# Kernel tuning notes

Hardware: AMD Instinct MI355X
Metric: run time of the kernel (lower is better)

## Reference

```python
import jax, jax.numpy as jnp
import numpy as np

N_HEADS = 16
HEAD_SIZE = 128  # n_embd // n_vq_heads = 2048 // 16
N_OPTIONS = 512


def setup_inputs() -> dict:
    key = jax.random.key(0)
    k1, k2, k3 = jax.random.split(key, 3)
    B, S, E = 4, 2048, N_HEADS * HEAD_SIZE
    x = jax.random.normal(k1, (B, S, E), dtype=jnp.float32)
    vq_head_weights = jax.random.normal(k2, (N_HEADS, N_OPTIONS, HEAD_SIZE), dtype=jnp.float32)
    vq_codebooks = jax.random.normal(k3, (N_HEADS, N_OPTIONS, HEAD_SIZE), dtype=jnp.float32)
    temperature = jnp.float32(1.0)
    return {
        "x": x,
        "vq_head_weights": vq_head_weights,
        "vq_codebooks": vq_codebooks,
        "temperature": temperature,
    }


def reference(x, vq_head_weights, vq_codebooks, temperature):
    # Training-mode forward of VQizer (softmax path).
    B, S, E = x.shape
    H, O, A = vq_head_weights.shape  # heads, options, head_size
    x_prepped = x.reshape(B, S, H, A)
    # per-head logits over codebook options
    logits = jnp.einsum('bsha,hoa->bsho', x_prepped, vq_head_weights)
    probs = jax.nn.softmax(logits / temperature, axis=-1)
    out = jnp.einsum('bsho,hoa->bsha', probs, vq_codebooks)
    return out.reshape(B, S, H * A)
```

## Files before the change

### kernel.cpp

```cpp
#include <hip/hip_runtime.h>
#include <math.h>

#define NHEADS 16
#define HS     128
#define NOPT   512
#define TB     128
#define OC     32
#define NCH    16
#define NITER  8
#define EMB    2048
#define LOG2E  1.44269504088896340736f
#define THRD   11.0f

typedef short bf16x8 __attribute__((ext_vector_type(8)));
typedef _Float16 f16x8 __attribute__((ext_vector_type(8)));
typedef unsigned short u16x8 __attribute__((ext_vector_type(8)));
typedef float f32x4 __attribute__((ext_vector_type(4)));
typedef float f32x16 __attribute__((ext_vector_type(16)));
typedef unsigned u32x4 __attribute__((ext_vector_type(4)));

__device__ __forceinline__ unsigned short f2bf(float f) {
    union { float f; unsigned u; } v; v.f = f;
    unsigned r = v.u + 0x7FFFu + ((v.u >> 16) & 1u);
    return (unsigned short)(r >> 16);
}
__device__ __forceinline__ float bf2f(unsigned short h) {
    union { unsigned u; float f; } v; v.u = ((unsigned)h) << 16;
    return v.f;
}
__device__ __forceinline__ unsigned short f2h(float f) {
    const _Float16 h = (_Float16)f;
    return __builtin_bit_cast(unsigned short, h);
}
__device__ __forceinline__ void gll16(const void* gptr, void* lptr) {
    __builtin_amdgcn_global_load_lds(
        (const __attribute__((address_space(1))) void*)gptr,
        (__attribute__((address_space(3))) void*)lptr,
        16, 0, 0);
}
__device__ __forceinline__ unsigned pkrtz(float lo, float hi) {
    unsigned r;
    asm("v_cvt_pkrtz_f16_f32 %0, %1, %2" : "=v"(r) : "v"(lo), "v"(hi));
    return r;
}
__device__ __forceinline__ void pl32swap(unsigned &a, unsigned &b) {
    asm volatile("v_permlane32_swap_b32 %0, %1" : "+v"(a), "+v"(b));
}
__device__ __forceinline__ f32x16 mfma32h(f16x8 a, f16x8 b, f32x16 c) {
    return __builtin_amdgcn_mfma_f32_32x32x16_f16(a, b, c, 0, 0, 0);
}

#define WCH    4096
#define CCH    4096
#define WS_C0  (NHEADS * NCH * WCH)
#define WS_TOTAL_BYTES ((size_t)(WS_C0 + NHEADS * NCH * CCH) * 2)

__global__ __launch_bounds__(256) void vq_prep(const float* __restrict__ W,
                                               const float* __restrict__ C,
                                               const float* __restrict__ temp,
                                               unsigned short* __restrict__ ws)
{
    const int b = blockIdx.x, t = threadIdx.x;
    if (b < NHEADS * NCH) {
        const float scW = (1.0f / temp[0]) * LOG2E;
        const float* src = W + (size_t)b * OC * HS;
        unsigned short* dst = ws + (size_t)b * WCH;
        for (int k = 0; k < 16; ++k) {
            const int e = k * 256 + t;
            const int opt = e >> 7, col = e & 127;
            dst[opt * 128 + (col ^ ((opt & 15) << 3))] = f2h(src[e] * scW);
        }
    } else {
        const int b2 = b - NHEADS * NCH;
        const float* src = C + (size_t)b2 * OC * HS;
        unsigned short* dst = ws + WS_C0 + (size_t)b2 * CCH;
        for (int k = 0; k < 16; ++k) {
            const int e = k * 256 + t;
            const int opt = e >> 7, a = e & 127;
            dst[a * 32 + (opt ^ (((a >> 1) & 3) << 3))] = f2h(src[e]);
        }
    }
}

__global__ __launch_bounds__(256, 2) void vq_main(
    const float* __restrict__ x, const unsigned short* __restrict__ ws,
    float* __restrict__ out)
{
    __shared__ unsigned short wbuf[2][2 * WCH];
    __shared__ unsigned short cbuf[2][2 * CCH];

    const int t = threadIdx.x, l = t & 63, w = t >> 6;
    const int la = l & 31, hf = l >> 5;
    const int b = blockIdx.x;
    const int head = ((b & 7) << 1) | ((b >> 3) & 1);
    const int n0 = (b >> 4) * TB;

    const char* gwbase = (const char*)(ws + (size_t)(head * NCH) * WCH);
    const char* gcbase = (const char*)(ws + WS_C0 + (size_t)(head * NCH) * CCH);

    {
        const char* gw = gwbase + w * 4096 + l * 16;
        char* lw = (char*)&wbuf[0][0] + w * 4096;
        const char* gc = gcbase + w * 4096 + l * 16;
        char* lc = (char*)&cbuf[0][0] + w * 4096;
        #pragma unroll
        for (int i = 0; i < 4; ++i) { gll16(gw + i * 1024, lw + i * 1024);
                                      gll16(gc + i * 1024, lc + i * 1024); }
    }

    f16x8 xf[8];
    {
        const float* xr = x + (size_t)(n0 + w * 32 + la) * EMB + head * HS + hf * 8;
        #pragma unroll
        for (int kb = 0; kb < 8; ++kb) {
            const float4 v0 = *(const float4*)(xr + kb * 16);
            const float4 v1 = *(const float4*)(xr + kb * 16 + 4);
            const float vv[8] = {v0.x, v0.y, v0.z, v0.w, v1.x, v1.y, v1.z, v1.w};
            u16x8 hh;
            #pragma unroll
            for (int j = 0; j < 8; ++j) hh[j] = f2h(vv[j]);
            xf[kb] = __builtin_bit_cast(f16x8, hh);
        }
    }

    f32x16 O0 = (f32x16)0.0f, O1 = (f32x16)0.0f, O2 = (f32x16)0.0f, O3 = (f32x16)0.0f;
    float M = -1.0e30f, sacc = 0.0f;

    asm volatile("s_waitcnt vmcnt(0)" ::: "memory");
    __builtin_amdgcn_s_barrier();

    for (int cc = 0; cc < NITER; ++cc) {
        const int cur = cc & 1;
        if (cc + 1 < NITER) {
            const char* gw = gwbase + (size_t)(cc + 1) * 16384 + w * 4096 + l * 16;
            char* lw = (char*)&wbuf[cur ^ 1][0] + w * 4096;
            const char* gc = gcbase + (size_t)(cc + 1) * 16384 + w * 4096 + l * 16;
            char* lc = (char*)&cbuf[cur ^ 1][0] + w * 4096;
            #pragma unroll
            for (int i = 0; i < 4; ++i) { gll16(gw + i * 1024, lw + i * 1024);
                                          gll16(gc + i * 1024, lc + i * 1024); }
        }

        f32x16 s0a = (f32x16)0.0f, s0b = (f32x16)0.0f;
        f32x16 s1a = (f32x16)0.0f, s1b = (f32x16)0.0f;
        const unsigned short* wb0 = &wbuf[cur][0];
        const unsigned short* wb1 = &wbuf[cur][WCH];
        #pragma unroll
        for (int kb = 0; kb < 8; ++kb) {
            const int idx = la * 128 + ((kb * 16 + hf * 8) ^ ((la & 15) << 3));
            const f16x8 w0 = *(const f16x8*)&wb0[idx];
            const f16x8 w1 = *(const f16x8*)&wb1[idx];
            if (kb & 1) { s0b = mfma32h(w0, xf[kb], s0b); s1b = mfma32h(w1, xf[kb], s1b); }
            else        { s0a = mfma32h(w0, xf[kb], s0a); s1a = mfma32h(w1, xf[kb], s1a); }
        }
        f32x16 S0 = s0a + s0b;
        f32x16 S1 = s1a + s1b;

        float cmax = fmaxf(S0[0], S1[0]);
        #pragma unroll
        for (int i = 1; i < 16; ++i) cmax = fmaxf(fmaxf(cmax, S0[i]), S1[i]);
        cmax = fmaxf(cmax, __shfl_xor(cmax, 32));
        if (__any(cmax > M + THRD)) {
            const float Mn = fmaxf(M, cmax);
            const float fr = exp2f(M - Mn);
            M = Mn;
            sacc *= fr;
            #pragma unroll
            for (int q = 0; q < 16; ++q) {
                const int row = (q & 3) + 8 * (q >> 2) + 4 * hf;
                const float f = __shfl(fr, row);
                O0[q] *= f; O1[q] *= f; O2[q] *= f; O3[q] *= f;
            }
        }
        #pragma unroll
        for (int q = 0; q < 16; ++q) { S0[q] = exp2f(S0[q] - M); S1[q] = exp2f(S1[q] - M); }
        {
            float s8[8];
            #pragma unroll
            for (int i = 0; i < 8; ++i)
                s8[i] = (S0[2 * i] + S0[2 * i + 1]) + (S1[2 * i] + S1[2 * i + 1]);
            sacc += ((s8[0] + s8[1]) + (s8[2] + s8[3])) +
                    ((s8[4] + s8[5]) + (s8[6] + s8[7]));
        }

        unsigned pk0 = pkrtz(S0[0],  S0[1]),  pk1 = pkrtz(S0[2],  S0[3]);
        unsigned pk2 = pkrtz(S0[4],  S0[5]),  pk3 = pkrtz(S0[6],  S0[7]);
        unsigned pk4 = pkrtz(S0[8],  S0[9]),  pk5 = pkrtz(S0[10], S0[11]);
        unsigned pk6 = pkrtz(S0[12], S0[13]), pk7 = pkrtz(S0[14], S0[15]);
        pl32swap(pk0, pk2); pl32swap(pk1, pk3);
        pl32swap(pk4, pk6); pl32swap(pk5, pk7);
        const f16x8 pa0 = __builtin_bit_cast(f16x8, (u32x4){pk0, pk1, pk2, pk3});
        const f16x8 pa1 = __builtin_bit_cast(f16x8, (u32x4){pk4, pk5, pk6, pk7});
        unsigned qk0 = pkrtz(S1[0],  S1[1]),  qk1 = pkrtz(S1[2],  S1[3]);
        unsigned qk2 = pkrtz(S1[4],  S1[5]),  qk3 = pkrtz(S1[6],  S1[7]);
        unsigned qk4 = pkrtz(S1[8],  S1[9]),  qk5 = pkrtz(S1[10], S1[11]);
        unsigned qk6 = pkrtz(S1[12], S1[13]), qk7 = pkrtz(S1[14], S1[15]);
        pl32swap(qk0, qk2); pl32swap(qk1, qk3);
        pl32swap(qk4, qk6); pl32swap(qk5, qk7);
        const f16x8 pa2 = __builtin_bit_cast(f16x8, (u32x4){qk0, qk1, qk2, qk3});
        const f16x8 pa3 = __builtin_bit_cast(f16x8, (u32x4){qk4, qk5, qk6, qk7});

        const unsigned short* cb0 = &cbuf[cur][0];
        const unsigned short* cb1 = &cbuf[cur][CCH];
        #pragma unroll
        for (int nt = 0; nt < 4; ++nt) {
            const int a = nt * 32 + la;
            const int sw = ((a >> 1) & 3) << 3;
            const int i0 = a * 32 + ((hf * 8) ^ sw);
            const int i1 = a * 32 + ((16 + hf * 8) ^ sw);
            f32x16& O = (nt == 0) ? O0 : (nt == 1) ? O1 : (nt == 2) ? O2 : O3;
            O = mfma32h(pa0, *(const f16x8*)&cb0[i0], O);
            O = mfma32h(pa1, *(const f16x8*)&cb0[i1], O);
            O = mfma32h(pa2, *(const f16x8*)&cb1[i0], O);
            O = mfma32h(pa3, *(const f16x8*)&cb1[i1], O);
        }

        asm volatile("s_waitcnt vmcnt(0)" ::: "memory");
        if (cc + 1 < NITER) __builtin_amdgcn_s_barrier();
    }

    const float stot = sacc + __shfl_xor(sacc, 32);
    const float rs = 1.0f / stot;
    #pragma unroll
    for (int q = 0; q < 16; ++q) {
        const int row = (q & 3) + 8 * (q >> 2) + 4 * hf;
        const float rq = __shfl(rs, row);
        float* op = out + (size_t)(n0 + w * 32 + row) * EMB + head * HS + la;
        op[0]  = O0[q] * rq;
        op[32] = O1[q] * rq;
        op[64] = O2[q] * rq;
        op[96] = O3[q] * rq;
    }
}

__global__ __launch_bounds__(256, 2) void vq_fwd_mfma(
    const float* __restrict__ x, const float* __restrict__ W,
    const float* __restrict__ C, const float* __restrict__ temp,
    float* __restrict__ out)
{
    __shared__ unsigned short xh_lds[64 * HS];
    __shared__ unsigned short xl_lds[64 * HS];
    __shared__ unsigned short wst[2][64 * HS];
    __shared__ unsigned short p_lds[4][16 * 64];

    const int t = threadIdx.x, l = t & 63, w = t >> 6, lr = l & 15, lk = l >> 4;
    const int b = blockIdx.x;
    const int h = ((b & 7) << 1) | ((b >> 3) & 1);
    const int n0 = (b >> 4) * 64;
    const float invT = 1.0f / temp[0];

    #pragma unroll
    for (int kk = 0; kk < 4; ++kk) {
        const int g = t + 256 * kk;
        const int row = g >> 4, c8 = (g & 15) * 8;
        const float* src = x + (size_t)(n0 + row) * EMB + h * HS + c8;
        const float4 v0 = *(const float4*)src;
        const float4 v1 = *(const float4*)(src + 4);
        float vv[8] = {v0.x, v0.y, v0.z, v0.w, v1.x, v1.y, v1.z, v1.w};
        u16x8 hh, ll;
        #pragma unroll
        for (int j = 0; j < 8; ++j) {
            const unsigned short hb = f2bf(vv[j]);
            hh[j] = hb; ll[j] = f2bf(vv[j] - bf2f(hb));
        }
        const int idx = row * HS + (c8 ^ ((row & 7) << 3));
        *(u16x8*)&xh_lds[idx] = hh;
        *(u16x8*)&xl_lds[idx] = ll;
    }

    f32x4 acc[32];
    #pragma unroll
    for (int i = 0; i < 32; ++i) acc[i] = f32x4{0.f, 0.f, 0.f, 0.f};
    bf16x8 axh[4], axl[4];

    #pragma unroll
    for (int c = 0; c < 8; ++c) {
        if (c) __syncthreads();
        #pragma unroll
        for (int kk = 0; kk < 4; ++kk) {
            const int g = t + 256 * kk;
            const int row = g >> 4, c8 = (g & 15) * 8;
            const float* src = W + ((size_t)h * NOPT + c * 64 + row) * HS + c8;
            const float4 v0 = *(const float4*)src;
            const float4 v1 = *(const float4*)(src + 4);
            float vv[8] = {v0.x, v0.y, v0.z, v0.w, v1.x, v1.y, v1.z, v1.w};
            u16x8 hh, ll;
            #pragma unroll
            for (int j = 0; j < 8; ++j) {
                const unsigned short hb = f2bf(vv[j]);
                hh[j] = hb; ll[j] = f2bf(vv[j] - bf2f(hb));
            }
            const int idx = row * HS + (c8 ^ ((row & 7) << 3));
            *(u16x8*)&wst[0][idx] = hh;
            *(u16x8*)&wst[1][idx] = ll;
        }
        __syncthreads();
        if (c == 0) {
            const int arow = w * 16 + lr;
            #pragma unroll
            for (int ks = 0; ks < 4; ++ks) {
                const int ai = arow * HS + ((lk * 8 + ks * 32) ^ ((arow & 7) << 3));
                axh[ks] = *(const bf16x8*)&xh_lds[ai];
                axl[ks] = *(const bf16x8*)&xl_lds[ai];
            }
        }
        #pragma unroll
        for (int nt = 0; nt < 4; ++nt) {
            const int brow = nt * 16 + lr;
            #pragma unroll
            for (int ks = 0; ks < 4; ++ks) {
                const int bi = brow * HS + ((lk * 8 + ks * 32) ^ ((brow & 7) << 3));
                const bf16x8 bh = *(const bf16x8*)&wst[0][bi];
                const bf16x8 bl = *(const bf16x8*)&wst[1][bi];
                acc[c*4+nt] = __builtin_amdgcn_mfma_f32_16x16x32_bf16(axh[ks], bh, acc[c*4+nt], 0, 0, 0);
                acc[c*4+nt] = __builtin_amdgcn_mfma_f32_16x16x32_bf16(axl[ks], bh, acc[c*4+nt], 0, 0, 0);
                acc[c*4+nt] = __builtin_amdgcn_mfma_f32_16x16x32_bf16(axh[ks], bl, acc[c*4+nt], 0, 0, 0);
            }
        }
    }

    float mx[4], rsn[4];
    #pragma unroll
    for (int r = 0; r < 4; ++r) {
        float m = -3.0e38f;
        #pragma unroll
        for (int i = 0; i < 32; ++i) m = fmaxf(m, acc[i][r]);
        m *= invT;
        #pragma unroll
        for (int s = 1; s < 16; s <<= 1) m = fmaxf(m, __shfl_xor(m, s));
        float sum = 0.f;
        #pragma unroll
        for (int i = 0; i < 32; ++i) sum += exp2f((acc[i][r] * invT - m) * LOG2E);
        #pragma unroll
        for (int s = 1; s < 16; s <<= 1) sum += __shfl_xor(sum, s);
        mx[r] = m; rsn[r] = 1.0f / sum;
    }

    f32x4 oacc[8];
    #pragma unroll
    for (int i = 0; i < 8; ++i) oacc[i] = f32x4{0.f, 0.f, 0.f, 0.f};
    const int pr_ = t & 31, ag = t >> 5;
    #pragma unroll
    for (int c = 0; c < 8; ++c) {
        __syncthreads();
        {
            const float* c0p = C + ((size_t)h * NOPT + c * 64 + 2 * pr_) * HS + ag * 16;
            float va[16], vb[16];
            #pragma unroll
            for (int q = 0; q < 4; ++q) {
                const float4 u0 = ((const float4*)c0p)[q];
                const float4 u1 = ((const float4*)(c0p + HS))[q];
                va[q*4+0] = u0.x; va[q*4+1] = u0.y; va[q*4+2] = u0.z; va[q*4+3] = u0.w;
                vb[q*4+0] = u1.x; vb[q*4+1] = u1.y; vb[q*4+2] = u1.z; vb[q*4+3] = u1.w;
            }
            unsigned* ct32 = (unsigned*)&wst[0][0];
            #pragma unroll
            for (int j = 0; j < 16; ++j) {
                const int a = ag * 16 + j;
                const unsigned pkv = (unsigned)f2bf(va[j]) | ((unsigned)f2bf(vb[j]) << 16);
                ct32[a * 32 + (pr_ ^ ((a & 7) << 2))] = pkv;
            }
        }
        #pragma unroll
        for (int nt = 0; nt < 4; ++nt) {
            #pragma unroll
            for (int r = 0; r < 4; ++r) {
                const float p = exp2f((acc[c*4+nt][r] * invT - mx[r]) * LOG2E);
                const int prow = lk * 4 + r;
                const int pcol = nt * 16 + lr;
                p_lds[w][prow * 64 + (pcol ^ ((prow & 7) << 3))] = f2bf(p);
            }
        }
        __syncthreads();
        #pragma unroll
        for (int ks = 0; ks < 2; ++ks) {
            const int ai = lr * 64 + ((lk * 8 + ks * 32) ^ ((lr & 7) << 3));
            const bf16x8 pa = *(const bf16x8*)&p_lds[w][ai];
            #pragma unroll
            for (int nt = 0; nt < 8; ++nt) {
                const int brow = nt * 16 + lr;
                const int bi = brow * 64 + ((lk * 8 + ks * 32) ^ ((brow & 7) << 3));
                const bf16x8 cbv = *(const bf16x8*)&wst[0][bi];
                oacc[nt] = __builtin_amdgcn_mfma_f32_16x16x32_bf16(pa, cbv, oacc[nt], 0, 0, 0);
            }
        }
    }

    #pragma unroll
    for (int nt = 0; nt < 8; ++nt) {
        #pragma unroll
        for (int r = 0; r < 4; ++r) {
            const int tok = n0 + w * 16 + lk * 4 + r;
            out[(size_t)tok * EMB + h * HS + nt * 16 + lr] = oacc[nt][r] * rsn[r];
        }
    }
}

extern "C" void kernel_launch(void* const* d_in, const int* in_sizes, int n_in,
                              void* d_out, int out_size, void* d_ws, size_t ws_size,
                              hipStream_t stream) {
    const float* x = (const float*)d_in[0];
    const float* W = (const float*)d_in[1];
    const float* C = (const float*)d_in[2];
    const float* T = (const float*)d_in[3];
    float* out     = (float*)d_out;

    const int ntok = in_sizes[0] / EMB;

    if (ws_size >= WS_TOTAL_BYTES) {
        hipLaunchKernelGGL(vq_prep, dim3(NHEADS * NCH * 2), dim3(256), 0, stream,
                           W, C, T, (unsigned short*)d_ws);
        const int nblk = (ntok / TB) * NHEADS;
        hipLaunchKernelGGL(vq_main, dim3(nblk), dim3(256), 0, stream,
                           x, (const unsigned short*)d_ws, out);
    } else {
        const int nblk = (ntok / 64) * NHEADS;
        hipLaunchKernelGGL(vq_fwd_mfma, dim3(nblk), dim3(256), 0, stream,
                           x, W, C, T, out);
    }
}
```

Measured before the change: 73.76 us.

## Load MFMA fragments directly from global in fragment-major layout, drop LDS staging

The prep kernel now writes the fp16 weight and codebook images in the exact per-lane fragment order the MFMA operands need, so each lane reads one contiguous 16-byte vector per operand. The main kernel drops the double-buffered LDS staging, the global-to-LDS loads and the per-iteration barriers, and reads fragments straight from global memory through the caches. This removes LDS traffic and synchronisation and frees LDS for occupancy. The cost is that every wave re-reads the same data from L1/L2, and load latency is no longer hidden by explicit prefetching.

```diff
diff --git a/kernel.cpp b/kernel.cpp
--- a/kernel.cpp
+++ b/kernel.cpp
@@ -32,12 +32,6 @@
     const _Float16 h = (_Float16)f;
     return __builtin_bit_cast(unsigned short, h);
 }
-__device__ __forceinline__ void gll16(const void* gptr, void* lptr) {
-    __builtin_amdgcn_global_load_lds(
-        (const __attribute__((address_space(1))) void*)gptr,
-        (__attribute__((address_space(3))) void*)lptr,
-        16, 0, 0);
-}
 __device__ __forceinline__ unsigned pkrtz(float lo, float hi) {
     unsigned r;
     asm("v_cvt_pkrtz_f16_f32 %0, %1, %2" : "=v"(r) : "v"(lo), "v"(hi));
@@ -50,10 +44,9 @@
     return __builtin_amdgcn_mfma_f32_32x32x16_f16(a, b, c, 0, 0, 0);
 }
 
-#define WCH    4096
-#define CCH    4096
-#define WS_C0  (NHEADS * NCH * WCH)
-#define WS_TOTAL_BYTES ((size_t)(WS_C0 + NHEADS * NCH * CCH) * 2)
+#define SUBELEMS 4096
+#define WS_C0  (NHEADS * NCH * SUBELEMS)
+#define WS_TOTAL_BYTES ((size_t)(WS_C0 + NHEADS * NCH * SUBELEMS) * 2)
 
 __global__ __launch_bounds__(256) void vq_prep(const float* __restrict__ W,
                                                const float* __restrict__ C,
@@ -64,20 +57,24 @@
     if (b < NHEADS * NCH) {
         const float scW = (1.0f / temp[0]) * LOG2E;
         const float* src = W + (size_t)b * OC * HS;
-        unsigned short* dst = ws + (size_t)b * WCH;
-        for (int k = 0; k < 16; ++k) {
-            const int e = k * 256 + t;
-            const int opt = e >> 7, col = e & 127;
-            dst[opt * 128 + (col ^ ((opt & 15) << 3))] = f2h(src[e] * scW);
+        unsigned short* dst = ws + (size_t)b * SUBELEMS;
+        for (int k4 = 0; k4 < 16; ++k4) {
+            const int e = k4 * 256 + t;
+            const int opt = e >> 7, k = e & 127;
+            const int kb = k >> 4, hf = (k >> 3) & 1, j = k & 7;
+            const int l = hf * 32 + opt;
+            dst[kb * 512 + l * 8 + j] = f2h(src[e] * scW);
         }
     } else {
         const int b2 = b - NHEADS * NCH;
         const float* src = C + (size_t)b2 * OC * HS;
-        unsigned short* dst = ws + WS_C0 + (size_t)b2 * CCH;
-        for (int k = 0; k < 16; ++k) {
-            const int e = k * 256 + t;
+        unsigned short* dst = ws + WS_C0 + (size_t)b2 * SUBELEMS;
+        for (int k4 = 0; k4 < 16; ++k4) {
+            const int e = k4 * 256 + t;
             const int opt = e >> 7, a = e & 127;
-            dst[a * 32 + (opt ^ (((a >> 1) & 3) << 3))] = f2h(src[e]);
+            const int q = opt >> 4, hf = (opt >> 3) & 1, j = opt & 7;
+            const int nt = a >> 5, l = hf * 32 + (a & 31);
+            dst[(nt * 2 + q) * 512 + l * 8 + j] = f2h(src[e]);
         }
     }
 }
@@ -86,27 +83,15 @@
     const float* __restrict__ x, const unsigned short* __restrict__ ws,
     float* __restrict__ out)
 {
-    __shared__ unsigned short wbuf[2][2 * WCH];
-    __shared__ unsigned short cbuf[2][2 * CCH];
-
     const int t = threadIdx.x, l = t & 63, w = t >> 6;
     const int la = l & 31, hf = l >> 5;
     const int b = blockIdx.x;
     const int head = ((b & 7) << 1) | ((b >> 3) & 1);
     const int n0 = (b >> 4) * TB;
 
-    const char* gwbase = (const char*)(ws + (size_t)(head * NCH) * WCH);
-    const char* gcbase = (const char*)(ws + WS_C0 + (size_t)(head * NCH) * CCH);
-
-    {
-        const char* gw = gwbase + w * 4096 + l * 16;
-        char* lw = (char*)&wbuf[0][0] + w * 4096;
-        const char* gc = gcbase + w * 4096 + l * 16;
-        char* lc = (char*)&cbuf[0][0] + w * 4096;
-        #pragma unroll
-        for (int i = 0; i < 4; ++i) { gll16(gw + i * 1024, lw + i * 1024);
-                                      gll16(gc + i * 1024, lc + i * 1024); }
-    }
+    const unsigned short* __restrict__ wimg = ws + (size_t)(head * NCH) * SUBELEMS;
+    const unsigned short* __restrict__ cimg = ws + WS_C0 + (size_t)(head * NCH) * SUBELEMS;
+    const int l8 = l * 8;
 
     f16x8 xf[8];
     {
@@ -126,30 +111,17 @@
     f32x16 O0 = (f32x16)0.0f, O1 = (f32x16)0.0f, O2 = (f32x16)0.0f, O3 = (f32x16)0.0f;
     float M = -1.0e30f, sacc = 0.0f;
 
-    asm volatile("s_waitcnt vmcnt(0)" ::: "memory");
-    __builtin_amdgcn_s_barrier();
-
     for (int cc = 0; cc < NITER; ++cc) {
-        const int cur = cc & 1;
-        if (cc + 1 < NITER) {
-            const char* gw = gwbase + (size_t)(cc + 1) * 16384 + w * 4096 + l * 16;
-            char* lw = (char*)&wbuf[cur ^ 1][0] + w * 4096;
-            const char* gc = gcbase + (size_t)(cc + 1) * 16384 + w * 4096 + l * 16;
-            char* lc = (char*)&cbuf[cur ^ 1][0] + w * 4096;
-            #pragma unroll
-            for (int i = 0; i < 4; ++i) { gll16(gw + i * 1024, lw + i * 1024);
-                                          gll16(gc + i * 1024, lc + i * 1024); }
-        }
+        const int sub0 = 2 * cc, sub1 = 2 * cc + 1;
 
         f32x16 s0a = (f32x16)0.0f, s0b = (f32x16)0.0f;
         f32x16 s1a = (f32x16)0.0f, s1b = (f32x16)0.0f;
-        const unsigned short* wb0 = &wbuf[cur][0];
-        const unsigned short* wb1 = &wbuf[cur][WCH];
+        const unsigned short* __restrict__ w0p = wimg + (size_t)sub0 * SUBELEMS;
+        const unsigned short* __restrict__ w1p = wimg + (size_t)sub1 * SUBELEMS;
         #pragma unroll
         for (int kb = 0; kb < 8; ++kb) {
-            const int idx = la * 128 + ((kb * 16 + hf * 8) ^ ((la & 15) << 3));
-            const f16x8 w0 = *(const f16x8*)&wb0[idx];
-            const f16x8 w1 = *(const f16x8*)&wb1[idx];
+            const f16x8 w0 = *(const f16x8*)&w0p[kb * 512 + l8];
+            const f16x8 w1 = *(const f16x8*)&w1p[kb * 512 + l8];
             if (kb & 1) { s0b = mfma32h(w0, xf[kb], s0b); s1b = mfma32h(w1, xf[kb], s1b); }
             else        { s0a = mfma32h(w0, xf[kb], s0a); s1a = mfma32h(w1, xf[kb], s1a); }
         }
@@ -200,23 +172,16 @@
         const f16x8 pa2 = __builtin_bit_cast(f16x8, (u32x4){qk0, qk1, qk2, qk3});
         const f16x8 pa3 = __builtin_bit_cast(f16x8, (u32x4){qk4, qk5, qk6, qk7});
 
-        const unsigned short* cb0 = &cbuf[cur][0];
-        const unsigned short* cb1 = &cbuf[cur][CCH];
+        const unsigned short* __restrict__ c0p = cimg + (size_t)sub0 * SUBELEMS;
+        const unsigned short* __restrict__ c1p = cimg + (size_t)sub1 * SUBELEMS;
         #pragma unroll
         for (int nt = 0; nt < 4; ++nt) {
-            const int a = nt * 32 + la;
-            const int sw = ((a >> 1) & 3) << 3;
-            const int i0 = a * 32 + ((hf * 8) ^ sw);
-            const int i1 = a * 32 + ((16 + hf * 8) ^ sw);
             f32x16& O = (nt == 0) ? O0 : (nt == 1) ? O1 : (nt == 2) ? O2 : O3;
-            O = mfma32h(pa0, *(const f16x8*)&cb0[i0], O);
-            O = mfma32h(pa1, *(const f16x8*)&cb0[i1], O);
-            O = mfma32h(pa2, *(const f16x8*)&cb1[i0], O);
-            O = mfma32h(pa3, *(const f16x8*)&cb1[i1], O);
-        }
-
-        asm volatile("s_waitcnt vmcnt(0)" ::: "memory");
-        if (cc + 1 < NITER) __builtin_amdgcn_s_barrier();
+            O = mfma32h(pa0, *(const f16x8*)&c0p[(nt * 2 + 0) * 512 + l8], O);
+            O = mfma32h(pa1, *(const f16x8*)&c0p[(nt * 2 + 1) * 512 + l8], O);
+            O = mfma32h(pa2, *(const f16x8*)&c1p[(nt * 2 + 0) * 512 + l8], O);
+            O = mfma32h(pa3, *(const f16x8*)&c1p[(nt * 2 + 1) * 512 + l8], O);
+        }
     }
 
     const float stot = sacc + __shfl_xor(sacc, 32);
```

Measured after the change: 95.43 us. +29.4%, slower.
